# Kernel tuning notes

Measured on AMD Instinct MI355X. Metric: run time of the kernel, lower is better.

Reference implementation:

```python
import jax, jax.numpy as jnp
import numpy as np

B, T, C = 2, 2048, 1024
N_HEAD = 16
HEAD_DIM = C // N_HEAD


def setup_inputs() -> dict:
    key = jax.random.key(0)
    k1, k2, k3 = jax.random.split(key, 3)
    x = jax.random.normal(k1, (B, T, C), dtype=jnp.float32)
    w_qkv = jax.random.normal(k2, (C, 3 * C), dtype=jnp.float32) * (C ** -0.5)
    w_proj = jax.random.normal(k3, (C, C), dtype=jnp.float32) * (C ** -0.5)
    b_proj = jnp.zeros((C,), dtype=jnp.float32)
    return {"x": x, "w_qkv": w_qkv, "w_proj": w_proj, "b_proj": b_proj}


def reference(x, w_qkv, w_proj, b_proj):
    Bx, Tx, Cx = x.shape
    # qkv projection: [B,T,3C] -> split into q,k,v each [B,H,T,D]
    qkv = x @ w_qkv  # [B,T,3C]
    qkv = qkv.reshape(Bx, Tx, 3, N_HEAD, HEAD_DIM)
    q = qkv[:, :, 0].transpose(0, 2, 1, 3)  # [B,H,T,D]
    k = qkv[:, :, 1].transpose(0, 2, 1, 3)
    v = qkv[:, :, 2].transpose(0, 2, 1, 3)
    scale = 1.0 / np.sqrt(HEAD_DIM).astype(np.float32)
    att = jnp.einsum('bhtd,bhsd->bhts', q, k) * scale  # [B,H,T,T]
    causal = jnp.tril(jnp.ones((Tx, Tx), dtype=bool))
    att = jnp.where(causal[None, None], att, -jnp.inf)
    att = jax.nn.softmax(att, axis=-1)
    # dropout p=0.0 -> identity (eval-mode math)
    y = jnp.einsum('bhts,bhsd->bhtd', att, v)  # [B,H,T,D]
    y = y.transpose(0, 2, 1, 3).reshape(Bx, Tx, Cx)
    return y @ w_proj + b_proj
```

## Files before the change

### kernel.cpp

```cpp
#include <hip/hip_runtime.h>

typedef __bf16 bf16x8 __attribute__((ext_vector_type(8)));
typedef float f32x4 __attribute__((ext_vector_type(4)));
typedef unsigned short u16;
typedef unsigned int u32;
typedef u32 u32x4 __attribute__((ext_vector_type(4)));
typedef u16 u16x8 __attribute__((ext_vector_type(8)));

#define B_ 2
#define T_ 2048
#define C_ 1024
#define H_ 16
#define D_ 64
#define QSCALE 0.18033688011112042f

__device__ __forceinline__ u16 f2bf(float f) {
    u32 u = __builtin_bit_cast(u32, f);
    u += 0x7fffu + ((u >> 16) & 1u);
    return (u16)(u >> 16);
}

__device__ __forceinline__ f32x4 mfma16(bf16x8 a, bf16x8 b, f32x4 c) {
    return __builtin_amdgcn_mfma_f32_16x16x32_bf16(a, b, c, 0, 0, 0);
}

__device__ __forceinline__ void gll16(const u16* g, u16* l) {
    __builtin_amdgcn_global_load_lds((const __attribute__((address_space(1))) unsigned int*)g,
                                     (__attribute__((address_space(3))) unsigned int*)l,
                                     16, 0, 0);
}

__global__ __launch_bounds__(256) void prep_kernel(const float* __restrict__ x,
                                                   const float* __restrict__ w_qkv,
                                                   const float* __restrict__ w_proj,
                                                   u16* __restrict__ x_bf,
                                                   u16* __restrict__ wqkv_t,
                                                   u16* __restrict__ wproj_t) {
    __shared__ float tile[64][65];
    int bid = blockIdx.x;
    int t = threadIdx.x;
    if (bid < 1024) {
        int base = bid * 4096 + t * 4;
#pragma unroll
        for (int it = 0; it < 4; ++it) {
            int i = base + it * 1024;
            float4 v = *(const float4*)(x + i);
            x_bf[i + 0] = f2bf(v.x);
            x_bf[i + 1] = f2bf(v.y);
            x_bf[i + 2] = f2bf(v.z);
            x_bf[i + 3] = f2bf(v.w);
        }
        return;
    }
    const float* in;
    u16* out;
    int N, tidx;
    if (bid < 1792) { in = w_qkv; out = wqkv_t; N = 3 * C_; tidx = bid - 1024; }
    else            { in = w_proj; out = wproj_t; N = C_;  tidx = bid - 1792; }
    int ntiles = N / 64;
    int n0 = (tidx % ntiles) * 64, k0 = (tidx / ntiles) * 64;
    int c = t & 63, r0 = t >> 6;
    for (int i = 0; i < 16; ++i) {
        int r = r0 * 16 + i;
        tile[r][c] = in[(size_t)(k0 + r) * N + n0 + c];
    }
    __syncthreads();
    for (int i = 0; i < 16; ++i) {
        int rn = r0 * 16 + i;
        out[(size_t)(n0 + rn) * C_ + k0 + c] = f2bf(tile[c][rn]);
    }
}

__global__ __launch_bounds__(256) void qkv_gemm(const u16* __restrict__ x_bf,
                                                const u16* __restrict__ wqkv_t,
                                                u16* __restrict__ Qo, u16* __restrict__ Ko,
                                                u16* __restrict__ Vto) {
    __shared__ __align__(16) u16 smem[16384];
    const int K = 1024;
    int bid = blockIdx.x;
    bool qk = (bid < 512);
    const u16 *A, *Bt;
    int m0, n0;
    if (qk) {
        A = x_bf; Bt = wqkv_t;
        n0 = (bid & 15) * 128; m0 = (bid >> 4) * 128;
    } else {
        int vb = bid - 512;
        A = wqkv_t + 2048 * 1024; Bt = x_bf;
        n0 = (vb & 31) * 128; m0 = (vb >> 5) * 128;
    }
    int t = threadIdx.x;
    int wave = t >> 6, lane = t & 63, lr = lane & 15, quad = lane >> 4;
    int wm = (wave >> 1) * 64, wn = (wave & 1) * 64;

    int srow = lane >> 2;
    int sgl = (lane & 3) ^ ((srow >> 1) & 3);
    int swz = (quad ^ ((lr >> 1) & 3)) * 8;

    f32x4 acc[4][4];
    for (int i = 0; i < 4; ++i)
        for (int j = 0; j < 4; ++j) acc[i][j] = (f32x4){0.f, 0.f, 0.f, 0.f};

    auto stage = [&](int b, int kb) {
        u16* As = smem + b * 4096;
        u16* Bs = smem + 8192 + b * 4096;
        for (int i = 0; i < 2; ++i) {
            int c = wave * 2 + i;
            int row = c * 16 + srow;
            gll16(&A[(size_t)(m0 + row) * K + kb + sgl * 8], &As[c * 512]);
            gll16(&Bt[(size_t)(n0 + row) * K + kb + sgl * 8], &Bs[c * 512]);
        }
    };

    stage(0, 0);
    for (int kt = 0; kt < 32; ++kt) {
        int buf = kt & 1;
        __syncthreads();
        if (kt < 31) stage(buf ^ 1, (kt + 1) * 32);
        const u16* As = smem + buf * 4096;
        const u16* Bs = smem + 8192 + buf * 4096;
        bf16x8 af[4], bfr[4];
        for (int mt = 0; mt < 4; ++mt)
            af[mt] = *(const bf16x8*)&As[(wm + mt * 16 + lr) * 32 + swz];
        for (int nt = 0; nt < 4; ++nt)
            bfr[nt] = *(const bf16x8*)&Bs[(wn + nt * 16 + lr) * 32 + swz];
        for (int mt = 0; mt < 4; ++mt)
            for (int nt = 0; nt < 4; ++nt) acc[mt][nt] = mfma16(af[mt], bfr[nt], acc[mt][nt]);
    }

    __syncthreads();
    u16* eb = smem + wave * 1152;
    int row = lane >> 2;
    int cb = (lane & 3) * 16;
    if (qk) {
        int colg = n0 + wn;
        int part = colg >> 10;
        int h = (colg & 1023) >> 6;
        float sc = (part == 0) ? QSCALE : 1.0f;
        u16* outb = (part == 0) ? Qo : Ko;
#pragma unroll
        for (int p = 0; p < 4; ++p) {
            asm volatile("" ::: "memory");
#pragma unroll
            for (int nt = 0; nt < 4; ++nt)
#pragma unroll
                for (int r = 0; r < 4; ++r)
                    eb[(quad * 4 + r) * 72 + nt * 16 + lr] = f2bf(acc[p][nt][r] * sc);
            asm volatile("" ::: "memory");
            u16x8 va = *(const u16x8*)(eb + row * 72 + cb);
            u16x8 vb = *(const u16x8*)(eb + row * 72 + cb + 8);
            asm volatile("" ::: "memory");
            int rowg = m0 + wm + p * 16 + row;
            int bb = rowg >> 11, tt = rowg & 2047;
            int bh = bb * H_ + h;
            u32* dst = (u32*)(outb + ((size_t)(bh * T_ + tt)) * D_ + cb);
            *(u32x4*)dst = __builtin_bit_cast(u32x4, va);
            *(u32x4*)(dst + 4) = __builtin_bit_cast(u32x4, vb);
        }
    } else {
#pragma unroll
        for (int p = 0; p < 4; ++p) {
            asm volatile("" ::: "memory");
#pragma unroll
            for (int nt = 0; nt < 4; ++nt)
#pragma unroll
                for (int r = 0; r < 4; ++r)
                    eb[(quad * 4 + r) * 72 + nt * 16 + lr] = f2bf(acc[p][nt][r]);
            asm volatile("" ::: "memory");
            u16x8 va = *(const u16x8*)(eb + row * 72 + cb);
            u16x8 vb = *(const u16x8*)(eb + row * 72 + cb + 8);
            asm volatile("" ::: "memory");
            int rowg = m0 + wm + p * 16 + row;
            int h = rowg >> 6, d = rowg & 63;
            int tg = n0 + wn + cb;
            int bb = tg >> 11, tt = tg & 2047;
            u32* dst = (u32*)(Vto + (((size_t)(bb * H_ + h)) * D_ + d) * T_ + tt);
            *(u32x4*)dst = __builtin_bit_cast(u32x4, va);
            *(u32x4*)(dst + 4) = __builtin_bit_cast(u32x4, vb);
        }
    }
}

__global__ __launch_bounds__(256) void gemm64_proj(const u16* __restrict__ A,
                                                   const u16* __restrict__ Bt,
                                                   float* __restrict__ Cout,
                                                   const float* __restrict__ bias,
                                                   int M, int N, int K) {
    __shared__ __align__(16) u16 smem[12288];
    int m0 = blockIdx.y * 128, n0 = blockIdx.x * 64;
    int t = threadIdx.x;
    int wave = t >> 6, lane = t & 63, lr = lane & 15, quad = lane >> 4;
    int srow = lane >> 2;
    int sgl = (lane & 3) ^ ((srow >> 1) & 3);
    int swz = (quad ^ ((lr >> 1) & 3)) * 8;

    f32x4 acc[2][4];
#pragma unroll
    for (int i = 0; i < 2; ++i)
#pragma unroll
        for (int j = 0; j < 4; ++j) acc[i][j] = (f32x4){0.f, 0.f, 0.f, 0.f};

    auto stage = [&](int b, int kb) {
        u16* As = smem + b * 4096;
        u16* Bs = smem + 8192 + b * 2048;
#pragma unroll
        for (int i = 0; i < 2; ++i) {
            int c = wave * 2 + i;
            int row = c * 16 + srow;
            gll16(&A[(size_t)(m0 + row) * K + kb + sgl * 8], &As[c * 512]);
        }
        {
            int row = wave * 16 + srow;
            gll16(&Bt[(size_t)(n0 + row) * K + kb + sgl * 8], &Bs[wave * 512]);
        }
    };

    int niter = K / 32;
    stage(0, 0);
    for (int kt = 0; kt < niter; ++kt) {
        int buf = kt & 1;
        __syncthreads();
        if (kt < niter - 1) stage(buf ^ 1, (kt + 1) * 32);
        const u16* As = smem + buf * 4096;
        const u16* Bs = smem + 8192 + buf * 2048;
        bf16x8 af[2], bfr[4];
#pragma unroll
        for (int mt = 0; mt < 2; ++mt)
            af[mt] = *(const bf16x8*)&As[(wave * 32 + mt * 16 + lr) * 32 + swz];
#pragma unroll
        for (int nt = 0; nt < 4; ++nt)
            bfr[nt] = *(const bf16x8*)&Bs[(nt * 16 + lr) * 32 + swz];
#pragma unroll
        for (int mt = 0; mt < 2; ++mt)
#pragma unroll
            for (int nt = 0; nt < 4; ++nt) acc[mt][nt] = mfma16(af[mt], bfr[nt], acc[mt][nt]);
    }

#pragma unroll
    for (int mt = 0; mt < 2; ++mt)
#pragma unroll
        for (int nt = 0; nt < 4; ++nt)
#pragma unroll
            for (int r = 0; r < 4; ++r) {
                int rowg = m0 + wave * 32 + mt * 16 + quad * 4 + r;
                int col = n0 + nt * 16 + lr;
                Cout[(size_t)rowg * N + col] = acc[mt][nt][r] + bias[col];
            }
}

__global__ __launch_bounds__(256, 4) void attn_kernel(const u16* __restrict__ Q,
                                                      const u16* __restrict__ Kb,
                                                      const u16* __restrict__ Vt,
                                                      u16* __restrict__ Y) {
    __shared__ __align__(16) u16 Kls[2][64 * 64];
    __shared__ __align__(16) u16 Vls[2][64 * 64];
    __shared__ __align__(16) u32 Pls[4][512];
    int qt = 31 - (blockIdx.x >> 5);
    int bh = blockIdx.x & 31;
    int t = threadIdx.x, wave = t >> 6, lane = t & 63, lr = lane & 15, quad = lane >> 4;

    const u16* kbase = Kb + (size_t)bh * (T_ * D_);
    const u16* vbase = Vt + (size_t)bh * (D_ * T_);
    const u16* Qg = Q + ((size_t)bh * T_ + qt * 64 + wave * 16 + lr) * D_;
    bf16x8 qfl = *(const bf16x8*)(Qg + quad * 8);
    bf16x8 qfh = *(const bf16x8*)(Qg + 32 + quad * 8);

    float lsum = 0.f;
    f32x4 o[4];
#pragma unroll
    for (int dt = 0; dt < 4; ++dt) o[dt] = (f32x4){0.f, 0.f, 0.f, 0.f};

    int srow = lane >> 3;
    int sgl = (lane & 7) ^ srow;
    int swz1 = (quad ^ (lr & 7)) * 8;
    int swz2 = ((quad + 4) ^ (lr & 7)) * 8;
    u32* pw = &Pls[wave][0];
    int pwbase = lr * 32 + (quad & 1) * 2;
    int rg1 = (quad ^ (lr & 7)) << 2;
    int rg2 = ((quad + 4) ^ (lr & 7)) << 2;

    for (int i = 0; i < 2; ++i) {
        int c = wave * 2 + i;
        int row = c * 8 + srow;
        gll16(kbase + (size_t)row * D_ + sgl * 8, &Kls[0][c * 512]);
        gll16(vbase + (size_t)row * T_ + sgl * 8, &Vls[0][c * 512]);
    }

    for (int kt = 0; kt <= qt; ++kt) {
        int buf = kt & 1;
        __syncthreads();
        if (kt < qt) {
            int nk = kt + 1;
            for (int i = 0; i < 2; ++i) {
                int c = wave * 2 + i;
                int row = c * 8 + srow;
                gll16(kbase + (size_t)(nk * 64 + row) * D_ + sgl * 8, &Kls[buf ^ 1][c * 512]);
                gll16(vbase + (size_t)row * T_ + nk * 64 + sgl * 8, &Vls[buf ^ 1][c * 512]);
            }
        }
        bf16x8 kf0[4], kf1[4], vf0[4], vf1[4];
#pragma unroll
        for (int st = 0; st < 4; ++st) {
            const u16* kp = &Kls[buf][(st * 16 + lr) * 64];
            kf0[st] = *(const bf16x8*)(kp + swz1);
            kf1[st] = *(const bf16x8*)(kp + swz2);
            const u16* vp = &Vls[buf][(st * 16 + lr) * 64];
            vf0[st] = *(const bf16x8*)(vp + swz1);
            vf1[st] = *(const bf16x8*)(vp + swz2);
        }
        f32x4 s[4];
        __builtin_amdgcn_s_setprio(1);
#pragma unroll
        for (int st = 0; st < 4; ++st) {
            s[st] = mfma16(kf0[st], qfl, (f32x4){0.f, 0.f, 0.f, 0.f});
            s[st] = mfma16(kf1[st], qfh, s[st]);
        }
        __builtin_amdgcn_s_setprio(0);
        if (kt == qt) {
            int qloc = wave * 16 + lr;
#pragma unroll
            for (int st = 0; st < 4; ++st)
#pragma unroll
                for (int r = 0; r < 4; ++r) {
                    if (st * 16 + quad * 4 + r > qloc) s[st][r] = -__builtin_inff();
                }
        }
        float sum = 0.f;
#pragma unroll
        for (int st = 0; st < 4; ++st)
#pragma unroll
            for (int r = 0; r < 4; ++r) {
                float p = __builtin_amdgcn_exp2f(s[st][r]);
                s[st][r] = p;
                sum += p;
            }
        sum += __shfl_xor(sum, 16);
        sum += __shfl_xor(sum, 32);
        lsum += sum;
        asm volatile("" ::: "memory");
#pragma unroll
        for (int st = 0; st < 4; ++st)
#pragma unroll
            for (int rp = 0; rp < 2; ++rp) {
                u32 lo = f2bf(s[st][2 * rp]);
                u32 hi = f2bf(s[st][2 * rp + 1]);
                pw[pwbase + (((st * 2 + (quad >> 1)) ^ (lr & 7)) << 2) + rp] = lo | (hi << 16);
            }
        asm volatile("" ::: "memory");
        const u32* prow = &pw[lr * 32];
        u32x4 plo = *(const u32x4*)(prow + rg1);
        u32x4 phi = *(const u32x4*)(prow + rg2);
        asm volatile("" ::: "memory");
        bf16x8 pfl = __builtin_bit_cast(bf16x8, plo);
        bf16x8 pfh = __builtin_bit_cast(bf16x8, phi);
        __builtin_amdgcn_s_setprio(1);
#pragma unroll
        for (int dt = 0; dt < 4; ++dt) {
            o[dt] = mfma16(vf0[dt], pfl, o[dt]);
            o[dt] = mfma16(vf1[dt], pfh, o[dt]);
        }
        __builtin_amdgcn_s_setprio(0);
    }

    int b = bh >> 4, h = bh & 15;
    float inv = 1.0f / lsum;
    asm volatile("" ::: "memory");
#pragma unroll
    for (int dt = 0; dt < 4; ++dt)
#pragma unroll
        for (int rp = 0; rp < 2; ++rp) {
            u32 lo = f2bf(o[dt][2 * rp] * inv);
            u32 hi = f2bf(o[dt][2 * rp + 1] * inv);
            pw[pwbase + (((dt * 2 + (quad >> 1)) ^ (lr & 7)) << 2) + rp] = lo | (hi << 16);
        }
    asm volatile("" ::: "memory");
    {
        int query = lane >> 2, wsel = lane & 3;
        const u32* prow = &pw[query * 32];
        u32x4 w0 = *(const u32x4*)(prow + (((wsel * 2) ^ (query & 7)) << 2));
        u32x4 w1 = *(const u32x4*)(prow + (((wsel * 2 + 1) ^ (query & 7)) << 2));
        u32* dst = (u32*)(Y + ((size_t)(b * T_ + qt * 64 + wave * 16 + query)) * C_ + h * 64 + wsel * 16);
        *(u32x4*)dst = w0;
        *(u32x4*)(dst + 4) = w1;
    }
}

extern "C" void kernel_launch(void* const* d_in, const int* in_sizes, int n_in,
                              void* d_out, int out_size, void* d_ws, size_t ws_size,
                              hipStream_t stream) {
    const float* x      = (const float*)d_in[0];
    const float* w_qkv  = (const float*)d_in[1];
    const float* w_proj = (const float*)d_in[2];
    const float* b_proj = (const float*)d_in[3];
    float* out = (float*)d_out;

    char* ws = (char*)d_ws;
    u16* x_bf    = (u16*)(ws + 0);
    u16* wqkv_t  = (u16*)(ws + 8388608);
    u16* wproj_t = (u16*)(ws + 14680064);
    u16* q_bf    = (u16*)(ws + 16777216);
    u16* k_bf    = (u16*)(ws + 25165824);
    u16* vt_bf   = (u16*)(ws + 33554432);
    u16* y_bf    = (u16*)(ws + 41943040);

    const int M = B_ * T_;

    prep_kernel<<<2048, 256, 0, stream>>>(x, w_qkv, w_proj, x_bf, wqkv_t, wproj_t);

    qkv_gemm<<<768, 256, 0, stream>>>(x_bf, wqkv_t, q_bf, k_bf, vt_bf);

    attn_kernel<<<32 * (T_ / 64), 256, 0, stream>>>(q_bf, k_bf, vt_bf, y_bf);

    gemm64_proj<<<dim3(C_ / 64, M / 128), 256, 0, stream>>>(
        y_bf, wproj_t, out, b_proj, M, C_, C_);
}
```

Before: 171.3 us.

## Use 256x256 tiles with quarter-staged pipelined prefetch in QKV GEMM

Enlarges the QKV GEMM block tile to 256x256 with 8 waves and a 64-wide k-step, and double-buffers LDS with an XOR swizzle. Next-tile global-to-LDS loads are split into four quarter stages, each placed between MFMA quarters and separated by barriers and explicit vmcnt waits, so memory traffic overlaps compute. This aims to raise data reuse per load and hide load latency. In exchange, the grid shrinks to 192 blocks, which can leave CUs idle, and register pressure and scheduling fragility go up.

```diff
diff --git a/kernel.cpp b/kernel.cpp
--- a/kernel.cpp
+++ b/kernel.cpp
@@ -71,64 +71,121 @@
     }
 }
 
-__global__ __launch_bounds__(256) void qkv_gemm(const u16* __restrict__ x_bf,
-                                                const u16* __restrict__ wqkv_t,
-                                                u16* __restrict__ Qo, u16* __restrict__ Ko,
-                                                u16* __restrict__ Vto) {
-    __shared__ __align__(16) u16 smem[16384];
+__global__ __launch_bounds__(512, 2) void qkv_gemm(const u16* __restrict__ x_bf,
+                                                   const u16* __restrict__ wqkv_t,
+                                                   u16* __restrict__ Qo, u16* __restrict__ Ko,
+                                                   u16* __restrict__ Vto) {
+    __shared__ __align__(16) u16 smem[65536];
     const int K = 1024;
     int bid = blockIdx.x;
-    bool qk = (bid < 512);
+    bool qk = (bid < 128);
     const u16 *A, *Bt;
     int m0, n0;
     if (qk) {
         A = x_bf; Bt = wqkv_t;
-        n0 = (bid & 15) * 128; m0 = (bid >> 4) * 128;
+        m0 = (bid >> 3) * 256; n0 = (bid & 7) * 256;
     } else {
-        int vb = bid - 512;
+        int vb = bid - 128;
         A = wqkv_t + 2048 * 1024; Bt = x_bf;
-        n0 = (vb & 31) * 128; m0 = (vb >> 5) * 128;
+        m0 = (vb >> 4) * 256; n0 = (vb & 15) * 256;
     }
     int t = threadIdx.x;
     int wave = t >> 6, lane = t & 63, lr = lane & 15, quad = lane >> 4;
-    int wm = (wave >> 1) * 64, wn = (wave & 1) * 64;
-
-    int srow = lane >> 2;
-    int sgl = (lane & 3) ^ ((srow >> 1) & 3);
-    int swz = (quad ^ ((lr >> 1) & 3)) * 8;
-
-    f32x4 acc[4][4];
-    for (int i = 0; i < 4; ++i)
+    int wave_m = wave >> 2, wave_n = wave & 3;
+    int wm = wave_m * 128, wn = wave_n * 64;
+
+    u16* As = smem;
+    u16* Bs = smem + 32768;
+
+    int gk = (((lane & 7) ^ ((lane >> 3) & 7))) * 8;
+    int srow8 = wave * 8 + (lane >> 3);
+
+    f32x4 acc[8][4];
+#pragma unroll
+    for (int i = 0; i < 8; ++i)
+#pragma unroll
         for (int j = 0; j < 4; ++j) acc[i][j] = (f32x4){0.f, 0.f, 0.f, 0.f};
 
-    auto stage = [&](int b, int kb) {
-        u16* As = smem + b * 4096;
-        u16* Bs = smem + 8192 + b * 4096;
-        for (int i = 0; i < 2; ++i) {
-            int c = wave * 2 + i;
-            int row = c * 16 + srow;
-            gll16(&A[(size_t)(m0 + row) * K + kb + sgl * 8], &As[c * 512]);
-            gll16(&Bt[(size_t)(n0 + row) * K + kb + sgl * 8], &Bs[c * 512]);
-        }
-    };
-
-    stage(0, 0);
-    for (int kt = 0; kt < 32; ++kt) {
+    auto stageA = [&](int buf, int kt, int h) {
+#pragma unroll
+        for (int j = 0; j < 2; ++j) {
+            int row = h * 128 + j * 64 + srow8;
+            gll16(&A[(size_t)(m0 + row) * K + kt * 64 + gk],
+                  &As[buf * 16384 + (h * 128 + j * 64 + wave * 8) * 64]);
+        }
+    };
+    auto stageB = [&](int buf, int kt, int h) {
+#pragma unroll
+        for (int j = 0; j < 2; ++j) {
+            int row = h * 128 + j * 64 + srow8;
+            gll16(&Bt[(size_t)(n0 + row) * K + kt * 64 + gk],
+                  &Bs[buf * 16384 + (h * 128 + j * 64 + wave * 8) * 64]);
+        }
+    };
+
+    bf16x8 aA[4][2], aB[4][2];
+    int kswz = ((lr & 7) << 3);
+    auto ldA = [&](int buf, int qm) {
+        const u16* p = &As[buf * 16384 + (wm + qm * 64) * 64];
+#pragma unroll
+        for (int mt = 0; mt < 4; ++mt)
+#pragma unroll
+            for (int kh = 0; kh < 2; ++kh)
+                aA[mt][kh] = *(const bf16x8*)&p[(mt * 16 + lr) * 64 + (((kh << 5) | (quad << 3)) ^ kswz)];
+    };
+    auto ldB = [&](int buf, int qn) {
+        const u16* p = &Bs[buf * 16384 + (wn + qn * 32) * 64];
+#pragma unroll
+        for (int nt = 0; nt < 2; ++nt)
+#pragma unroll
+            for (int kh = 0; kh < 2; ++kh)
+                aB[qn * 2 + nt][kh] = *(const bf16x8*)&p[(nt * 16 + lr) * 64 + (((kh << 5) | (quad << 3)) ^ kswz)];
+    };
+    auto mfmaQ = [&](int qm, int qn) {
+        __builtin_amdgcn_s_setprio(1);
+#pragma unroll
+        for (int kh = 0; kh < 2; ++kh)
+#pragma unroll
+            for (int mt = 0; mt < 4; ++mt)
+#pragma unroll
+                for (int nt = 0; nt < 2; ++nt)
+                    acc[qm * 4 + mt][qn * 2 + nt] =
+                        mfma16(aA[mt][kh], aB[qn * 2 + nt][kh], acc[qm * 4 + mt][qn * 2 + nt]);
+        __builtin_amdgcn_s_setprio(0);
+    };
+
+    stageA(0, 0, 0); stageA(0, 0, 1); stageB(0, 0, 0); stageB(0, 0, 1);
+
+    for (int kt = 0; kt < 16; ++kt) {
         int buf = kt & 1;
-        __syncthreads();
-        if (kt < 31) stage(buf ^ 1, (kt + 1) * 32);
-        const u16* As = smem + buf * 4096;
-        const u16* Bs = smem + 8192 + buf * 4096;
-        bf16x8 af[4], bfr[4];
-        for (int mt = 0; mt < 4; ++mt)
-            af[mt] = *(const bf16x8*)&As[(wm + mt * 16 + lr) * 32 + swz];
-        for (int nt = 0; nt < 4; ++nt)
-            bfr[nt] = *(const bf16x8*)&Bs[(wn + nt * 16 + lr) * 32 + swz];
-        for (int mt = 0; mt < 4; ++mt)
-            for (int nt = 0; nt < 4; ++nt) acc[mt][nt] = mfma16(af[mt], bfr[nt], acc[mt][nt]);
-    }
-
-    __syncthreads();
+        bool pf = (kt < 15);
+        __builtin_amdgcn_s_barrier();
+        asm volatile("" ::: "memory");
+        if (pf) stageA(buf ^ 1, kt + 1, 0);
+        if (pf) asm volatile("s_waitcnt vmcnt(2)" ::: "memory");
+        else    asm volatile("s_waitcnt vmcnt(0)" ::: "memory");
+        __builtin_amdgcn_sched_barrier(0);
+        ldA(buf, 0); ldB(buf, 0);
+        mfmaQ(0, 0);
+        __builtin_amdgcn_s_barrier();
+        asm volatile("" ::: "memory");
+        if (pf) stageA(buf ^ 1, kt + 1, 1);
+        ldB(buf, 1);
+        mfmaQ(0, 1);
+        __builtin_amdgcn_s_barrier();
+        asm volatile("" ::: "memory");
+        if (pf) stageB(buf ^ 1, kt + 1, 0);
+        ldA(buf, 1);
+        mfmaQ(1, 1);
+        __builtin_amdgcn_s_barrier();
+        asm volatile("" ::: "memory");
+        if (pf) stageB(buf ^ 1, kt + 1, 1);
+        mfmaQ(1, 0);
+    }
+
+    __builtin_amdgcn_s_barrier();
+    asm volatile("" ::: "memory");
+
     u16* eb = smem + wave * 1152;
     int row = lane >> 2;
     int cb = (lane & 3) * 16;
@@ -139,7 +196,7 @@
         float sc = (part == 0) ? QSCALE : 1.0f;
         u16* outb = (part == 0) ? Qo : Ko;
 #pragma unroll
-        for (int p = 0; p < 4; ++p) {
+        for (int p = 0; p < 8; ++p) {
             asm volatile("" ::: "memory");
 #pragma unroll
             for (int nt = 0; nt < 4; ++nt)
@@ -159,7 +216,7 @@
         }
     } else {
 #pragma unroll
-        for (int p = 0; p < 4; ++p) {
+        for (int p = 0; p < 8; ++p) {
             asm volatile("" ::: "memory");
 #pragma unroll
             for (int nt = 0; nt < 4; ++nt)
@@ -407,7 +464,7 @@
 
     prep_kernel<<<2048, 256, 0, stream>>>(x, w_qkv, w_proj, x_bf, wqkv_t, wproj_t);
 
-    qkv_gemm<<<768, 256, 0, stream>>>(x_bf, wqkv_t, q_bf, k_bf, vt_bf);
+    qkv_gemm<<<192, 512, 0, stream>>>(x_bf, wqkv_t, q_bf, k_bf, vt_bf);
 
     attn_kernel<<<32 * (T_ / 64), 256, 0, stream>>>(q_bf, k_bf, vt_bf, y_bf);
 
```

Result: faster. 167.7 us (-2.1%).
